# Performance work log

Hardware: AMD Instinct MI355X
Metric: run time of the kernel (lower is better)

Reference implementation:

```python
import jax, jax.numpy as jnp
import numpy as np

LEVELS = (4, 3, 2, 1)
EMBED = 4096


def _spp(x):
    # adaptive max pool to n x n per level (H,W divisible by every level), concat
    N, C, H, W = x.shape
    feats = []
    for n in LEVELS:
        p = x.reshape(N, C, n, H // n, n, W // n).max(axis=(3, 5))
        feats.append(p.reshape(N, C * n * n))
    return jnp.concatenate(feats, axis=1)  # (N, 90)


def _lstm_cell(x, h, c, wih, whh, bih, bhh):
    # torch gate order: i, f, g, o
    g = x @ wih.T + bih + h @ whh.T + bhh
    i, f, gg, o = jnp.split(g, 4, axis=-1)
    c2 = jax.nn.sigmoid(f) * c + jax.nn.sigmoid(i) * jnp.tanh(gg)
    h2 = jax.nn.sigmoid(o) * jnp.tanh(c2)
    return h2, c2


def _lin_init(key, out_d, in_d):
    k = 1.0 / np.sqrt(in_d)
    kw, kb = jax.random.split(key)
    w = jax.random.uniform(kw, (out_d, in_d), jnp.float32, -k, k)
    b = jax.random.uniform(kb, (out_d,), jnp.float32, -k, k)
    return w, b


def setup_inputs() -> dict:
    key = jax.random.key(0)
    ks = jax.random.split(key, 9)
    frames = jax.random.normal(ks[0], (8, 256, 3, 96, 96), jnp.float32)
    spp_fc_w, spp_fc_b = _lin_init(ks[1], EMBED, 90)
    fc7_w, fc7_b = _lin_init(ks[2], 64, EMBED)
    forecast_w, forecast_b = _lin_init(ks[3], 90, 32)
    fc8_w, fc8_b = _lin_init(ks[4], 1, 32)
    lstm1_wih, lstm1_bih = _lin_init(ks[5], 256, 64)
    lstm1_whh, lstm1_bhh = _lin_init(ks[6], 256, 64)
    lstm2_wih, lstm2_bih = _lin_init(ks[7], 128, 64)
    lstm2_whh, lstm2_bhh = _lin_init(ks[8], 128, 32)
    return dict(frames=frames, spp_fc_w=spp_fc_w, spp_fc_b=spp_fc_b,
                fc7_w=fc7_w, fc7_b=fc7_b,
                lstm1_wih=lstm1_wih, lstm1_whh=lstm1_whh, lstm1_bih=lstm1_bih, lstm1_bhh=lstm1_bhh,
                lstm2_wih=lstm2_wih, lstm2_whh=lstm2_whh, lstm2_bih=lstm2_bih, lstm2_bhh=lstm2_bhh,
                forecast_w=forecast_w, forecast_b=forecast_b, fc8_w=fc8_w, fc8_b=fc8_b)


def reference(frames, spp_fc_w, spp_fc_b, fc7_w, fc7_b,
              lstm1_wih, lstm1_whh, lstm1_bih, lstm1_bhh,
              lstm2_wih, lstm2_whh, lstm2_bih, lstm2_bhh,
              forecast_w, forecast_b, fc8_w, fc8_b):
    B, S, C, H, W = frames.shape
    pooled = _spp(frames.reshape(B * S, C, H, W))               # (B*S, 90)
    emb = jax.nn.relu(pooled @ spp_fc_w.T + spp_fc_b)           # (B*S, 4096)
    emb = jax.nn.relu(emb @ fc7_w.T + fc7_b).reshape(B, S, -1)  # (B, S, 64)

    def step(carry, e):
        h1, c1, h2, c2 = carry
        h1n, c1n = _lstm_cell(e, h1, c1, lstm1_wih, lstm1_whh, lstm1_bih, lstm1_bhh)
        h2n, c2n = _lstm_cell(h1n, h2, c2, lstm2_wih, lstm2_whh, lstm2_bih, lstm2_bhh)
        fpool = h2n @ forecast_w.T + forecast_b                  # (B, 90)
        fe = jax.nn.relu(fpool @ spp_fc_w.T + spp_fc_b)
        fe = jax.nn.relu(fe @ fc7_w.T + fc7_b)
        fh1, _ = _lstm_cell(fe, h1n, c1n, lstm1_wih, lstm1_whh, lstm1_bih, lstm1_bhh)
        fh2, _ = _lstm_cell(fh1, h2n, c2n, lstm2_wih, lstm2_whh, lstm2_bih, lstm2_bhh)
        return (h1n, c1n, h2n, c2n), (h2n, fh2, fpool)

    z = lambda d: jnp.zeros((B, d), frames.dtype)
    init = (z(64), z(64), z(32), z(32))
    _, (prog, fprog, fpooled) = jax.lax.scan(step, init, jnp.swapaxes(emb, 0, 1))
    prog = jnp.swapaxes(prog, 0, 1)        # (B, S, 32)
    fprog = jnp.swapaxes(fprog, 0, 1)      # (B, S, 32)
    fpooled = jnp.swapaxes(fpooled, 0, 1)  # (B, S, 90)
    progress = jax.nn.sigmoid(prog @ fc8_w.T + fc8_b)[..., 0]    # (B, S)
    fprogress = jax.nn.sigmoid(fprog @ fc8_w.T + fc8_b)[..., 0]  # (B, S)
    return (progress, fprogress, pooled.reshape(B, S, -1), fpooled)
```

## Files before the change

### kernel.cpp

```cpp
#include <hip/hip_runtime.h>
#include <math.h>

static const size_t OFF_POOLED = 0;
static const size_t OFF_EMB1   = 184320;
static const size_t OFF_ACC1   = OFF_EMB1 + 8388608;
static const size_t OFF_ACC2   = OFF_ACC1 + 131072;
static const size_t OFF_X1     = OFF_ACC2 + 131072;
static const size_t OFF_FPOOL  = OFF_X1 + 524288;
static const size_t OFF_H1     = OFF_FPOOL + 184320;
static const size_t OFF_C1     = OFF_H1 + 131072;
static const size_t OFF_H2     = OFF_C1 + 131072;
static const size_t OFF_C2     = OFF_H2 + 65536;

typedef _Float16 h2f_t __attribute__((ext_vector_type(2)));

__device__ __forceinline__ float fsig(float x) {
    return __builtin_amdgcn_rcpf(1.0f + __expf(-x));
}
__device__ __forceinline__ float ftanh(float x) {
    return 1.0f - 2.0f * __builtin_amdgcn_rcpf(__expf(2.0f * x) + 1.0f);
}

__device__ __forceinline__ float fdot2(h2f_t a, h2f_t b, float c) {
#if __has_builtin(__builtin_amdgcn_fdot2)
    return __builtin_amdgcn_fdot2(a, b, c, false);
#else
    return c + (float)a.x * (float)b.x + (float)a.y * (float)b.y;
#endif
}
__device__ __forceinline__ h2f_t h2pack(float x, float y) {
    h2f_t r; r.x = (_Float16)x; r.y = (_Float16)y; return r;
}
__device__ __forceinline__ h2f_t h2bits(int v) {
    return __builtin_bit_cast(h2f_t, v);
}
__device__ __forceinline__ void lds_fence() {
    asm volatile("s_waitcnt lgkmcnt(0)" ::: "memory");
}
__device__ __forceinline__ void permswap(float& x, float& y) {
    asm volatile("v_permlane32_swap_b32 %0, %1" : "+v"(x), "+v"(y));
}

__global__ __launch_bounds__(256) void spp_kernel(const float* __restrict__ frames,
                                                  float* __restrict__ out_pooled,
                                                  float* __restrict__ ws_pooled) {
    __shared__ __align__(16) float img[9216];
    __shared__ float p4[16], p3[9];
    int blk = blockIdx.x;
    int n = blk / 3, c = blk % 3;
    const float* src = frames + (size_t)blk * 9216;
    int tid = threadIdx.x;
    const float4* s4 = (const float4*)src;
    float4* i4 = (float4*)img;
#pragma unroll
    for (int j = 0; j < 9; ++j) i4[tid + 256 * j] = s4[tid + 256 * j];
    __syncthreads();
    {
        int r = tid >> 4, i = tid & 15;
        int ri = r >> 2, rj = r & 3;
        const float* base = &img[(24 * ri) * 96 + 24 * rj];
        float m = -3.402823466e38f;
#pragma unroll 6
        for (int k = 0; k < 36; ++k) {
            int e = i + 16 * k;
            int row = e / 24;
            int col = e - row * 24;
            m = fmaxf(m, base[row * 96 + col]);
        }
#pragma unroll
        for (int sh = 8; sh >= 1; sh >>= 1) m = fmaxf(m, __shfl_xor(m, sh));
        if (i == 0) p4[r] = m;
    }
    if (tid < 144) {
        int r = tid >> 4, i = tid & 15;
        int ri = r / 3, rj = r % 3;
        const float* base = &img[(32 * ri) * 96 + 32 * rj];
        float m = -3.402823466e38f;
#pragma unroll 8
        for (int k = 0; k < 64; ++k) {
            int e = i + 16 * k;
            int row = e >> 5, col = e & 31;
            m = fmaxf(m, base[row * 96 + col]);
        }
#pragma unroll
        for (int sh = 8; sh >= 1; sh >>= 1) m = fmaxf(m, __shfl_xor(m, sh));
        if (i == 0) p3[r] = m;
    }
    __syncthreads();
    if (tid < 30) {
        float v; int off;
        if (tid < 16) { v = p4[tid]; off = c * 16 + tid; }
        else if (tid < 25) { int q = tid - 16; v = p3[q]; off = 48 + c * 9 + q; }
        else if (tid < 29) {
            int q = tid - 25; int i2 = q >> 1, j2 = q & 1;
            v = fmaxf(fmaxf(p4[(2 * i2) * 4 + 2 * j2], p4[(2 * i2) * 4 + 2 * j2 + 1]),
                      fmaxf(p4[(2 * i2 + 1) * 4 + 2 * j2], p4[(2 * i2 + 1) * 4 + 2 * j2 + 1]));
            off = 75 + c * 4 + q;
        } else {
            float m = p4[0];
#pragma unroll
            for (int q = 1; q < 16; ++q) m = fmaxf(m, p4[q]);
            v = m; off = 87 + c;
        }
        out_pooled[(size_t)n * 90 + off] = v;
        ws_pooled[(size_t)n * 90 + off] = v;
    }
}

__global__ __launch_bounds__(256) void gemm90_kernel(const float* __restrict__ X,
                                                     const float* __restrict__ W,
                                                     const float* __restrict__ bias,
                                                     float* __restrict__ Y) {
    __shared__ __align__(16) float Xs[32][132];
    __shared__ __align__(16) float Ws[32][132];
    int tid = threadIdx.x;
    int R0 = blockIdx.x * 128, C0 = blockIdx.y * 128;
    int r0t = (tid >> 4) * 8, c0t = (tid & 15) * 8;
    float acc[8][8];
#pragma unroll
    for (int i = 0; i < 8; ++i)
// ... 68 lines not shown
    __shared__ __align__(16) float Xs[32][132];
    __shared__ __align__(16) float Ws[32][68];
    int tid = threadIdx.x;
    int R0 = blockIdx.x * 128;
    int K0 = blockIdx.y * 256;
    int r0t = (tid >> 4) * 8, c0t = (tid & 15) * 4;
    float acc[8][4];
#pragma unroll
    for (int i = 0; i < 8; ++i)
#pragma unroll
        for (int j = 0; j < 4; ++j) acc[i][j] = 0.f;

    for (int k0 = K0; k0 < K0 + 256; k0 += 32) {
#pragma unroll
        for (int j = 0; j < 4; ++j) {
            int idx = tid + 256 * j;
            int row = idx & 127, q = idx >> 7;
            float4 a = *(const float4*)&X[(size_t)(R0 + row) * 4096 + k0 + 4 * q];
            Xs[4 * q + 0][row] = a.x; Xs[4 * q + 1][row] = a.y;
            Xs[4 * q + 2][row] = a.z; Xs[4 * q + 3][row] = a.w;
        }
#pragma unroll
        for (int j = 0; j < 2; ++j) {
            int idx = tid + 256 * j;
            int col = idx & 63, q = idx >> 6;
            float4 a = *(const float4*)&W[(size_t)col * 4096 + k0 + 4 * q];
            Ws[4 * q + 0][col] = a.x; Ws[4 * q + 1][col] = a.y;
            Ws[4 * q + 2][col] = a.z; Ws[4 * q + 3][col] = a.w;
        }
        __syncthreads();
#pragma unroll 8
        for (int kk = 0; kk < 32; ++kk) {
            float4 xa = *(const float4*)&Xs[kk][r0t];
            float4 xb = *(const float4*)&Xs[kk][r0t + 4];
            float4 wa = *(const float4*)&Ws[kk][c0t];
            float xr[8] = {xa.x, xa.y, xa.z, xa.w, xb.x, xb.y, xb.z, xb.w};
            float wc[4] = {wa.x, wa.y, wa.z, wa.w};
#pragma unroll
            for (int i = 0; i < 8; ++i)
#pragma unroll
                for (int j = 0; j < 4; ++j) acc[i][j] += xr[i] * wc[j];
        }
        __syncthreads();
    }
#pragma unroll
    for (int i = 0; i < 8; ++i)
#pragma unroll
        for (int j = 0; j < 4; ++j)
            atomicAdd(&acc_out[(size_t)(R0 + r0t + i) * 64 + c0t + j], acc[i][j]);
}

__global__ __launch_bounds__(256) void x1_kernel(const float* __restrict__ acc1,
                                                 const float* __restrict__ fc7_b,
                                                 const float* __restrict__ wih1,
                                                 const float* __restrict__ bih1,
                                                 const float* __restrict__ bhh1,
                                                 float* __restrict__ X1) {
    __shared__ __align__(16) float xr[8][64];
    int tid = threadIdx.x;
    int R0 = blockIdx.x * 8;
#pragma unroll
    for (int j = 0; j < 2; ++j) {
        int idx = tid + 256 * j;
        int r = idx >> 6, k = idx & 63;
        xr[r][k] = fmaxf(acc1[(size_t)(R0 + r) * 64 + k] + fc7_b[k], 0.f);
    }
    __syncthreads();
    int u = tid;
    float w[64];
#pragma unroll
    for (int q = 0; q < 16; ++q) {
        float4 a = *(const float4*)&wih1[(size_t)u * 64 + 4 * q];
        w[4 * q] = a.x; w[4 * q + 1] = a.y; w[4 * q + 2] = a.z; w[4 * q + 3] = a.w;
    }
    float bias = bih1[u] + bhh1[u];
    for (int r = 0; r < 8; ++r) {
        float g = bias;
#pragma unroll
        for (int k = 0; k < 64; ++k) g += w[k] * xr[r][k];
        X1[(size_t)(R0 + r) * 256 + u] = g;
    }
}

__global__ __launch_bounds__(128, 1) void seq_kernel(const float* __restrict__ X1,
                                                     const float* __restrict__ whh1,
                                                     const float* __restrict__ wih2,
                                                     const float* __restrict__ whh2,
                                                     const float* __restrict__ bih2,
                                                     const float* __restrict__ bhh2,
                                                     float* __restrict__ h1_all, float* __restrict__ c1_all,
                                                     float* __restrict__ h2_all, float* __restrict__ c2_all) {
    __shared__ __align__(16) _Float16 h1h[2][64];
    __shared__ __align__(16) _Float16 h2h[32];
    const int tid = threadIdx.x;
    const int l = tid & 63;
    const size_t n0 = (size_t)blockIdx.x * 256;
    const float* xp = X1 + n0 * 256;

    if (tid < 64) {
        h2f_t w1[4][32];
#pragma unroll
        for (int g = 0; g < 4; ++g) {
            const float* wr = whh1 + (size_t)(g * 64 + l) * 64;
#pragma unroll
            for (int q = 0; q < 32; ++q) w1[g][q] = h2pack(wr[2 * q], wr[2 * q + 1]);
        }
        float c1;
        {
            float a0 = xp[l], a1 = xp[64 + l], a2 = xp[128 + l], a3 = xp[192 + l];
            (void)a1;
            c1 = fsig(a0) * ftanh(a2);
            float h1n = fsig(a3) * ftanh(c1);
            h1h[0][l] = (_Float16)h1n;
            h1_all[n0 * 64 + l] = h1n;
            c1_all[n0 * 64 + l] = c1;
        }
        float xb0[4], xb1[4];
        {
            const float* x1r = xp + 256;
            xb0[0] = x1r[l]; xb0[1] = x1r[64 + l]; xb0[2] = x1r[128 + l]; xb0[3] = x1r[192 + l];
            const float* x2r = xp + 512;
            xb1[0] = x2r[l]; xb1[1] = x2r[64 + l]; xb1[2] = x2r[128 + l]; xb1[3] = x2r[192 + l];
        }
        lds_fence();
        int4 hv[8];
        {
            const int4* hb = (const int4*)&h1h[0][0];
#pragma unroll
            for (int q = 0; q < 8; ++q) hv[q] = hb[q];
        }
        __builtin_amdgcn_s_barrier();

#pragma unroll 2
        for (int t = 0; t < 256; ++t) {
            float* xc = (t & 1) ? xb1 : xb0;
            float a0 = xc[0], a1 = xc[1], a2 = xc[2], a3 = xc[3];
            {
                int tr = (t + 3 < 256) ? (t + 3) : 255;
                const float* xq = xp + (size_t)tr * 256;
                xc[0] = xq[l]; xc[1] = xq[64 + l]; xc[2] = xq[128 + l]; xc[3] = xq[192 + l];
            }
            float b0 = 0.f, b1 = 0.f, b2 = 0.f, b3 = 0.f;
#pragma unroll
            for (int q = 0; q < 8; ++q) {
                int4 v = hv[q];
                h2f_t hh0 = h2bits(v.x), hh1 = h2bits(v.y), hh2 = h2bits(v.z), hh3 = h2bits(v.w);
                a0 = fdot2(w1[0][4 * q], hh0, a0);     a1 = fdot2(w1[1][4 * q], hh0, a1);
                a2 = fdot2(w1[2][4 * q], hh0, a2);     a3 = fdot2(w1[3][4 * q], hh0, a3);
                b0 = fdot2(w1[0][4 * q + 1], hh1, b0); b1 = fdot2(w1[1][4 * q + 1], hh1, b1);
                b2 = fdot2(w1[2][4 * q + 1], hh1, b2); b3 = fdot2(w1[3][4 * q + 1], hh1, b3);
                a0 = fdot2(w1[0][4 * q + 2], hh2, a0); a1 = fdot2(w1[1][4 * q + 2], hh2, a1);
                a2 = fdot2(w1[2][4 * q + 2], hh2, a2); a3 = fdot2(w1[3][4 * q + 2], hh2, a3);
                b0 = fdot2(w1[0][4 * q + 3], hh3, b0); b1 = fdot2(w1[1][4 * q + 3], hh3, b1);
                b2 = fdot2(w1[2][4 * q + 3], hh3, b2); b3 = fdot2(w1[3][4 * q + 3], hh3, b3);
            }
            a0 += b0; a1 += b1; a2 += b2; a3 += b3;
            c1 = fsig(a1) * c1 + fsig(a0) * ftanh(a2);
            float h1n = fsig(a3) * ftanh(c1);
            h1h[(t + 1) & 1][l] = (_Float16)h1n;
            if (t < 255) {
                h1_all[(n0 + t + 1) * 64 + l] = h1n;
                c1_all[(n0 + t + 1) * 64 + l] = c1;
            }
            {
                const int4* hb = (const int4*)&h1h[(t + 1) & 1][0];
#pragma unroll
                for (int q = 0; q < 8; ++q) hv[q] = hb[q];
            }
            asm volatile("s_waitcnt lgkmcnt(8)" ::: "memory");
            __builtin_amdgcn_s_barrier();
        }
    } else {
        h2f_t w2a[2][32], w2b[2][16];
#pragma unroll
        for (int g = 0; g < 2; ++g) {
            const float* wa = wih2 + (size_t)(g * 64 + l) * 64;
#pragma unroll
            for (int q = 0; q < 32; ++q) w2a[g][q] = h2pack(wa[2 * q], wa[2 * q + 1]);
            const float* wb = whh2 + (size_t)(g * 64 + l) * 32;
#pragma unroll
            for (int q = 0; q < 16; ++q) w2b[g][q] = h2pack(wb[2 * q], wb[2 * q + 1]);
        }
        const float b2a = bih2[l] + bhh2[l];
        const float b2b = bih2[64 + l] + bhh2[64 + l];
        const bool hi = (l >= 32);
        if (l < 32) h2h[l] = (_Float16)0.f;
        lds_fence();
        int4 gv[4];
        {
            const int4* gb = (const int4*)&h2h[0];
#pragma unroll
            for (int q = 0; q < 4; ++q) gv[q] = gb[q];
        }
        float c2 = 0.f;
        __builtin_amdgcn_s_barrier();

        for (int t = 0; t < 256; ++t) {
            int4 hv[8];
            {
                const int4* hb = (const int4*)&h1h[t & 1][0];
#pragma unroll
                for (int q = 0; q < 8; ++q) hv[q] = hb[q];
            }
            float pa = b2a, pb = b2b, pc = 0.f, pd = 0.f;
            float pe = 0.f, pf = 0.f, pg = 0.f, ph = 0.f;
#pragma unroll
            for (int q = 0; q < 4; ++q) {
                int4 u = gv[q];
                h2f_t gg0 = h2bits(u.x), gg1 = h2bits(u.y), gg2 = h2bits(u.z), gg3 = h2bits(u.w);
                pe = fdot2(w2b[0][4 * q], gg0, pe);     pf = fdot2(w2b[1][4 * q], gg0, pf);
                pg = fdot2(w2b[0][4 * q + 1], gg1, pg); ph = fdot2(w2b[1][4 * q + 1], gg1, ph);
                pe = fdot2(w2b[0][4 * q + 2], gg2, pe); pf = fdot2(w2b[1][4 * q + 2], gg2, pf);
                pg = fdot2(w2b[0][4 * q + 3], gg3, pg); ph = fdot2(w2b[1][4 * q + 3], gg3, ph);
            }
#pragma unroll
            for (int q = 0; q < 8; ++q) {
                int4 v = hv[q];
                h2f_t hh0 = h2bits(v.x), hh1 = h2bits(v.y), hh2 = h2bits(v.z), hh3 = h2bits(v.w);
                pa = fdot2(w2a[0][4 * q], hh0, pa);     pb = fdot2(w2a[1][4 * q], hh0, pb);
                pa = fdot2(w2a[0][4 * q + 1], hh1, pa); pb = fdot2(w2a[1][4 * q + 1], hh1, pb);
                pc = fdot2(w2a[0][4 * q + 2], hh2, pc); pd = fdot2(w2a[1][4 * q + 2], hh2, pd);
                pc = fdot2(w2a[0][4 * q + 3], hh3, pc); pd = fdot2(w2a[1][4 * q + 3], hh3, pd);
            }
            pa = (pa + pc) + (pe + pg);
            pb = (pb + pd) + (pf + ph);
            float s1a = pa, s1b = pb;
            permswap(s1a, s1b);
            float s2a = pb, s2b = pa;
            permswap(s2a, s2b);
            float gi = hi ? s2a : s1a;
            float gf = hi ? s2b : s1b;
            float gg = hi ? s1a : s2a;
            float go = hi ? s1b : s2b;
            c2 = fsig(gf) * c2 + fsig(gi) * ftanh(gg);
            float h2n = fsig(go) * ftanh(c2);
            if (l < 32) {
                h2h[l] = (_Float16)h2n;
                h2_all[(n0 + t) * 32 + l] = h2n;
                c2_all[(n0 + t) * 32 + l] = c2;
            }
            lds_fence();
            {
                const int4* gb = (const int4*)&h2h[0];
#pragma unroll
                for (int q = 0; q < 4; ++q) gv[q] = gb[q];
            }
            __builtin_amdgcn_s_barrier();
        }
    }
}

__global__ __launch_bounds__(256) void fpool_kernel(const float* __restrict__ h2_all,
                                                    const float* __restrict__ fw,
                                                    const float* __restrict__ fb,
                                                    const float* __restrict__ fc8_w,
                                                    const float* __restrict__ fc8_b,
                                                    float* __restrict__ fpool_ws,
                                                    float* __restrict__ out_fpooled,
                                                    float* __restrict__ out_progress) {
    __shared__ __align__(16) float h2t[16][32];
    __shared__ float fwl[2880];
    int tid = threadIdx.x;
    int R0 = blockIdx.x * 16;
#pragma unroll
    for (int j = 0; j < 2; ++j) {
        int idx = tid + 256 * j;
        int r = idx >> 5, k = idx & 31;
        h2t[r][k] = h2_all[(size_t)(R0 + r) * 32 + k];
    }
    for (int idx = tid; idx < 2880; idx += 256) fwl[idx] = fw[idx];
    __syncthreads();
    for (int j = 0; j < 6; ++j) {
        int idx = tid + 256 * j;
        if (idx < 1440) {
            int r = idx / 90, cc = idx % 90;
            float g = fb[cc];
#pragma unroll
            for (int k = 0; k < 32; ++k) g += h2t[r][k] * fwl[cc * 32 + k];
            fpool_ws[(size_t)(R0 + r) * 90 + cc] = g;
            out_fpooled[(size_t)(R0 + r) * 90 + cc] = g;
        }
    }
    if (tid < 16) {
        float g = fc8_b[0];
#pragma unroll
        for (int k = 0; k < 32; ++k) g += h2t[tid][k] * fc8_w[k];
        out_progress[R0 + tid] = fsig(g);
    }
}

__global__ __launch_bounds__(256) void fh_kernel(const float* __restrict__ acc2,
                                                 const float* __restrict__ fc7_b,
                                                 const float* __restrict__ h1_all,
                                                 const float* __restrict__ c1_all,
                                                 const float* __restrict__ h2_all,
                                                 const float* __restrict__ c2_all,
                                                 const float* __restrict__ wih1,
                                                 const float* __restrict__ whh1,
                                                 const float* __restrict__ bih1,
                                                 const float* __restrict__ bhh1,
                                                 const float* __restrict__ wih2,
                                                 const float* __restrict__ whh2,
                                                 const float* __restrict__ bih2,
                                                 const float* __restrict__ bhh2,
                                                 const float* __restrict__ fc8_w,
                                                 const float* __restrict__ fc8_b,
                                                 float* __restrict__ out_fprog) {
    __shared__ __align__(16) float xcat[8][128];
    __shared__ float g1f[8][256];
    __shared__ __align__(16) float x2c[8][96];
    __shared__ float g2f[8][128];
    __shared__ __align__(16) float fh2s[8][32];
    int tid = threadIdx.x;
    int R0 = blockIdx.x * 8;
#pragma unroll
    for (int j = 0; j < 4; ++j) {
        int idx = tid + 256 * j;
        int r = idx >> 7, k = idx & 127;
        float v;
        if (k < 64) v = fmaxf(acc2[(size_t)(R0 + r) * 64 + k] + fc7_b[k], 0.f);
        else v = h1_all[(size_t)(R0 + r) * 64 + (k - 64)];
        xcat[r][k] = v;
    }
    {
        int r = tid >> 5, k = tid & 31;
        x2c[r][64 + k] = h2_all[(size_t)(R0 + r) * 32 + k];
    }
    __syncthreads();
    {
        int u = tid;
// ... 32 lines not shown
        float wa[64], wb2[32];
#pragma unroll
        for (int q = 0; q < 16; ++q) {
            float4 a = *(const float4*)&wih2[(size_t)u * 64 + 4 * q];
            wa[4 * q] = a.x; wa[4 * q + 1] = a.y; wa[4 * q + 2] = a.z; wa[4 * q + 3] = a.w;
        }
#pragma unroll
        for (int q = 0; q < 8; ++q) {
            float4 b = *(const float4*)&whh2[(size_t)u * 32 + 4 * q];
            wb2[4 * q] = b.x; wb2[4 * q + 1] = b.y; wb2[4 * q + 2] = b.z; wb2[4 * q + 3] = b.w;
        }
        float bias = bih2[u] + bhh2[u];
        for (int r = rb; r < rb + 4; ++r) {
            float g = bias;
#pragma unroll
            for (int k = 0; k < 64; ++k) g += wa[k] * x2c[r][k];
#pragma unroll
            for (int k = 0; k < 32; ++k) g += wb2[k] * x2c[r][64 + k];
            g2f[r][u] = g;
        }
    }
    __syncthreads();
    {
        int r = tid >> 5, v = tid & 31;
        float gi = g2f[r][v], gf = g2f[r][32 + v], gg = g2f[r][64 + v], go = g2f[r][96 + v];
        float c2v = c2_all[(size_t)(R0 + r) * 32 + v];
        float c = fsig(gf) * c2v + fsig(gi) * ftanh(gg);
        fh2s[r][v] = fsig(go) * ftanh(c);
    }
    __syncthreads();
    if (tid < 8) {
        float g = fc8_b[0];
#pragma unroll
        for (int k = 0; k < 32; ++k) g += fh2s[tid][k] * fc8_w[k];
        out_fprog[R0 + tid] = fsig(g);
    }
}

extern "C" void kernel_launch(void* const* d_in, const int* in_sizes, int n_in,
                              void* d_out, int out_size, void* d_ws, size_t ws_size,
                              hipStream_t stream) {
    (void)in_sizes; (void)n_in; (void)out_size; (void)ws_size;
    const float* frames   = (const float*)d_in[0];
    const float* spp_fc_w = (const float*)d_in[1];
    const float* spp_fc_b = (const float*)d_in[2];
    const float* fc7_w    = (const float*)d_in[3];
    const float* fc7_b    = (const float*)d_in[4];
    const float* l1_wih   = (const float*)d_in[5];
    const float* l1_whh   = (const float*)d_in[6];
    const float* l1_bih   = (const float*)d_in[7];
    const float* l1_bhh   = (const float*)d_in[8];
    const float* l2_wih   = (const float*)d_in[9];
    const float* l2_whh   = (const float*)d_in[10];
    const float* l2_bih   = (const float*)d_in[11];
    const float* l2_bhh   = (const float*)d_in[12];
    const float* fo_w     = (const float*)d_in[13];
    const float* fo_b     = (const float*)d_in[14];
    const float* fc8_w    = (const float*)d_in[15];
    const float* fc8_b    = (const float*)d_in[16];
    float* out = (float*)d_out;
    float* ws  = (float*)d_ws;

    float* pooled = ws + OFF_POOLED;
    float* emb1   = ws + OFF_EMB1;
    float* acc1   = ws + OFF_ACC1;
    float* acc2   = ws + OFF_ACC2;
    float* X1     = ws + OFF_X1;
    float* fpool  = ws + OFF_FPOOL;
    float* h1a    = ws + OFF_H1;
    float* c1a    = ws + OFF_C1;
    float* h2a    = ws + OFF_H2;
    float* c2a    = ws + OFF_C2;

    float* out_prog    = out;
    float* out_fprog   = out + 2048;
    float* out_pooled  = out + 4096;
    float* out_fpooled = out + 188416;

    hipMemsetAsync(acc1, 0, (size_t)262144 * sizeof(float), stream);
    spp_kernel<<<6144, 256, 0, stream>>>(frames, out_pooled, pooled);
    gemm90_kernel<<<dim3(16, 32), 256, 0, stream>>>(pooled, spp_fc_w, spp_fc_b, emb1);
    gemmk_kernel<<<dim3(16, 16), 256, 0, stream>>>(emb1, fc7_w, acc1);
    x1_kernel<<<256, 256, 0, stream>>>(acc1, fc7_b, l1_wih, l1_bih, l1_bhh, X1);
    seq_kernel<<<8, 128, 0, stream>>>(X1, l1_whh, l2_wih, l2_whh, l2_bih, l2_bhh, h1a, c1a, h2a, c2a);
    fpool_kernel<<<128, 256, 0, stream>>>(h2a, fo_w, fo_b, fc8_w, fc8_b, fpool, out_fpooled, out_prog);
    gemm90_kernel<<<dim3(16, 32), 256, 0, stream>>>(fpool, spp_fc_w, spp_fc_b, emb1);
    gemmk_kernel<<<dim3(16, 16), 256, 0, stream>>>(emb1, fc7_w, acc2);
    fh_kernel<<<256, 256, 0, stream>>>(acc2, fc7_b, h1a, c1a, h2a, c2a,
                                       l1_wih, l1_whh, l1_bih, l1_bhh,
                                       l2_wih, l2_whh, l2_bih, l2_bhh,
                                       fc8_w, fc8_b, out_fprog);
}
```

Before: 669.5 us.

## Split LSTM recurrence dot products across four waves with LDS partial sums

Result: slower. 723.9 us (+8.1%).

```diff
diff --git a/kernel.cpp b/kernel.cpp
--- a/kernel.cpp
+++ b/kernel.cpp
@@ -270,7 +270,7 @@
     }
 }
 
-__global__ __launch_bounds__(128, 1) void seq_kernel(const float* __restrict__ X1,
+__global__ __launch_bounds__(256, 1) void seq_kernel(const float* __restrict__ X1,
                                                      const float* __restrict__ whh1,
                                                      const float* __restrict__ wih2,
                                                      const float* __restrict__ whh2,
@@ -280,23 +280,25 @@
                                                      float* __restrict__ h2_all, float* __restrict__ c2_all) {
     __shared__ __align__(16) _Float16 h1h[2][64];
     __shared__ __align__(16) _Float16 h2h[32];
+    __shared__ __align__(16) float p1[64][4];
+    __shared__ __align__(16) float p2[64][2];
     const int tid = threadIdx.x;
+    const int wid = tid >> 6;
     const int l = tid & 63;
     const size_t n0 = (size_t)blockIdx.x * 256;
     const float* xp = X1 + n0 * 256;
 
-    if (tid < 64) {
-        h2f_t w1[4][32];
+    if (wid == 0) {
+        h2f_t w1c[4][12];
 #pragma unroll
         for (int g = 0; g < 4; ++g) {
             const float* wr = whh1 + (size_t)(g * 64 + l) * 64;
 #pragma unroll
-            for (int q = 0; q < 32; ++q) w1[g][q] = h2pack(wr[2 * q], wr[2 * q + 1]);
+            for (int q = 0; q < 12; ++q) w1c[g][q] = h2pack(wr[2 * q], wr[2 * q + 1]);
         }
         float c1;
         {
-            float a0 = xp[l], a1 = xp[64 + l], a2 = xp[128 + l], a3 = xp[192 + l];
-            (void)a1;
+            float a0 = xp[l], a2 = xp[128 + l], a3 = xp[192 + l];
             c1 = fsig(a0) * ftanh(a2);
             float h1n = fsig(a3) * ftanh(c1);
             h1h[0][l] = (_Float16)h1n;
@@ -311,14 +313,13 @@
             xb1[0] = x2r[l]; xb1[1] = x2r[64 + l]; xb1[2] = x2r[128 + l]; xb1[3] = x2r[192 + l];
         }
         lds_fence();
-        int4 hv[8];
+        __builtin_amdgcn_s_barrier();
+        int4 hv[3];
         {
             const int4* hb = (const int4*)&h1h[0][0];
 #pragma unroll
-            for (int q = 0; q < 8; ++q) hv[q] = hb[q];
-        }
-        __builtin_amdgcn_s_barrier();
-
+            for (int q = 0; q < 3; ++q) hv[q] = hb[q];
+        }
 #pragma unroll 2
         for (int t = 0; t < 256; ++t) {
             float* xc = (t & 1) ? xb1 : xb0;
@@ -330,19 +331,21 @@
             }
             float b0 = 0.f, b1 = 0.f, b2 = 0.f, b3 = 0.f;
 #pragma unroll
-            for (int q = 0; q < 8; ++q) {
+            for (int q = 0; q < 3; ++q) {
                 int4 v = hv[q];
                 h2f_t hh0 = h2bits(v.x), hh1 = h2bits(v.y), hh2 = h2bits(v.z), hh3 = h2bits(v.w);
-                a0 = fdot2(w1[0][4 * q], hh0, a0);     a1 = fdot2(w1[1][4 * q], hh0, a1);
-                a2 = fdot2(w1[2][4 * q], hh0, a2);     a3 = fdot2(w1[3][4 * q], hh0, a3);
-                b0 = fdot2(w1[0][4 * q + 1], hh1, b0); b1 = fdot2(w1[1][4 * q + 1], hh1, b1);
-                b2 = fdot2(w1[2][4 * q + 1], hh1, b2); b3 = fdot2(w1[3][4 * q + 1], hh1, b3);
-                a0 = fdot2(w1[0][4 * q + 2], hh2, a0); a1 = fdot2(w1[1][4 * q + 2], hh2, a1);
-                a2 = fdot2(w1[2][4 * q + 2], hh2, a2); a3 = fdot2(w1[3][4 * q + 2], hh2, a3);
-                b0 = fdot2(w1[0][4 * q + 3], hh3, b0); b1 = fdot2(w1[1][4 * q + 3], hh3, b1);
-                b2 = fdot2(w1[2][4 * q + 3], hh3, b2); b3 = fdot2(w1[3][4 * q + 3], hh3, b3);
-            }
-            a0 += b0; a1 += b1; a2 += b2; a3 += b3;
+                a0 = fdot2(w1c[0][4 * q], hh0, a0);     a1 = fdot2(w1c[1][4 * q], hh0, a1);
+                a2 = fdot2(w1c[2][4 * q], hh0, a2);     a3 = fdot2(w1c[3][4 * q], hh0, a3);
+                b0 = fdot2(w1c[0][4 * q + 1], hh1, b0); b1 = fdot2(w1c[1][4 * q + 1], hh1, b1);
+                b2 = fdot2(w1c[2][4 * q + 1], hh1, b2); b3 = fdot2(w1c[3][4 * q + 1], hh1, b3);
+                a0 = fdot2(w1c[0][4 * q + 2], hh2, a0); a1 = fdot2(w1c[1][4 * q + 2], hh2, a1);
+                a2 = fdot2(w1c[2][4 * q + 2], hh2, a2); a3 = fdot2(w1c[3][4 * q + 2], hh2, a3);
+                b0 = fdot2(w1c[0][4 * q + 3], hh3, b0); b1 = fdot2(w1c[1][4 * q + 3], hh3, b1);
+                b2 = fdot2(w1c[2][4 * q + 3], hh3, b2); b3 = fdot2(w1c[3][4 * q + 3], hh3, b3);
+            }
+            __builtin_amdgcn_s_barrier();
+            float4 p = *(const float4*)&p1[l][0];
+            a0 += b0 + p.x; a1 += b1 + p.y; a2 += b2 + p.z; a3 += b3 + p.w;
             c1 = fsig(a1) * c1 + fsig(a0) * ftanh(a2);
             float h1n = fsig(a3) * ftanh(c1);
             h1h[(t + 1) & 1][l] = (_Float16)h1n;
@@ -353,65 +356,93 @@
             {
                 const int4* hb = (const int4*)&h1h[(t + 1) & 1][0];
 #pragma unroll
-                for (int q = 0; q < 8; ++q) hv[q] = hb[q];
-            }
-            asm volatile("s_waitcnt lgkmcnt(8)" ::: "memory");
+                for (int q = 0; q < 3; ++q) hv[q] = hb[q];
+            }
+            asm volatile("s_waitcnt lgkmcnt(3)" ::: "memory");
             __builtin_amdgcn_s_barrier();
         }
-    } else {
-        h2f_t w2a[2][32], w2b[2][16];
+    } else if (wid == 1) {
+        h2f_t w1c[4][20];
+#pragma unroll
+        for (int g = 0; g < 4; ++g) {
+            const float* wr = whh1 + (size_t)(g * 64 + l) * 64 + 24;
+#pragma unroll
+            for (int q = 0; q < 20; ++q) w1c[g][q] = h2pack(wr[2 * q], wr[2 * q + 1]);
+        }
+        __builtin_amdgcn_s_barrier();
+        int4 hv[5];
+        {
+            const int4* hb = (const int4*)&h1h[0][0];
+#pragma unroll
+            for (int q = 0; q < 5; ++q) hv[q] = hb[q + 3];
+        }
+        for (int t = 0; t < 256; ++t) {
+            float a0 = 0.f, a1 = 0.f, a2 = 0.f, a3 = 0.f;
+            float b0 = 0.f, b1 = 0.f, b2 = 0.f, b3 = 0.f;
+#pragma unroll
+            for (int q = 0; q < 5; ++q) {
+                int4 v = hv[q];
+                h2f_t hh0 = h2bits(v.x), hh1 = h2bits(v.y), hh2 = h2bits(v.z), hh3 = h2bits(v.w);
+                a0 = fdot2(w1c[0][4 * q], hh0, a0);     a1 = fdot2(w1c[1][4 * q], hh0, a1);
+                a2 = fdot2(w1c[2][4 * q], hh0, a2);     a3 = fdot2(w1c[3][4 * q], hh0, a3);
+                b0 = fdot2(w1c[0][4 * q + 1], hh1, b0); b1 = fdot2(w1c[1][4 * q + 1], hh1, b1);
+                b2 = fdot2(w1c[2][4 * q + 1], hh1, b2); b3 = fdot2(w1c[3][4 * q + 1], hh1, b3);
+                a0 = fdot2(w1c[0][4 * q + 2], hh2, a0); a1 = fdot2(w1c[1][4 * q + 2], hh2, a1);
+                a2 = fdot2(w1c[2][4 * q + 2], hh2, a2); a3 = fdot2(w1c[3][4 * q + 2], hh2, a3);
+                b0 = fdot2(w1c[0][4 * q + 3], hh3, b0); b1 = fdot2(w1c[1][4 * q + 3], hh3, b1);
+                b2 = fdot2(w1c[2][4 * q + 3], hh3, b2); b3 = fdot2(w1c[3][4 * q + 3], hh3, b3);
+            }
+            float4 pw;
+            pw.x = a0 + b0; pw.y = a1 + b1; pw.z = a2 + b2; pw.w = a3 + b3;
+            *(float4*)&p1[l][0] = pw;
+            lds_fence();
+            __builtin_amdgcn_s_barrier();
+            __builtin_amdgcn_s_barrier();
+            {
+                const int4* hb = (const int4*)&h1h[(t + 1) & 1][0];
+#pragma unroll
+                for (int q = 0; q < 5; ++q) hv[q] = hb[q + 3];
+            }
+        }
+    } else if (wid == 2) {
+        h2f_t w2a[2][4], w2b[2][4];
 #pragma unroll
         for (int g = 0; g < 2; ++g) {
             const float* wa = wih2 + (size_t)(g * 64 + l) * 64;
 #pragma unroll
-            for (int q = 0; q < 32; ++q) w2a[g][q] = h2pack(wa[2 * q], wa[2 * q + 1]);
+            for (int q = 0; q < 4; ++q) w2a[g][q] = h2pack(wa[2 * q], wa[2 * q + 1]);
             const float* wb = whh2 + (size_t)(g * 64 + l) * 32;
 #pragma unroll
-            for (int q = 0; q < 16; ++q) w2b[g][q] = h2pack(wb[2 * q], wb[2 * q + 1]);
+            for (int q = 0; q < 4; ++q) w2b[g][q] = h2pack(wb[2 * q], wb[2 * q + 1]);
         }
         const float b2a = bih2[l] + bhh2[l];
         const float b2b = bih2[64 + l] + bhh2[64 + l];
         const bool hi = (l >= 32);
-        if (l < 32) h2h[l] = (_Float16)0.f;
-        lds_fence();
-        int4 gv[4];
-        {
-            const int4* gb = (const int4*)&h2h[0];
-#pragma unroll
-            for (int q = 0; q < 4; ++q) gv[q] = gb[q];
-        }
         float c2 = 0.f;
+        int4 gv; gv.x = 0; gv.y = 0; gv.z = 0; gv.w = 0;
         __builtin_amdgcn_s_barrier();
-
+        int4 hv = ((const int4*)&h1h[0][0])[0];
         for (int t = 0; t < 256; ++t) {
-            int4 hv[8];
+            float pe = 0.f, pf = 0.f, pg_ = 0.f, ph = 0.f;
             {
-                const int4* hb = (const int4*)&h1h[t & 1][0];
-#pragma unroll
-                for (int q = 0; q < 8; ++q) hv[q] = hb[q];
+                h2f_t gg0 = h2bits(gv.x), gg1 = h2bits(gv.y), gg2 = h2bits(gv.z), gg3 = h2bits(gv.w);
+                pe = fdot2(w2b[0][0], gg0, pe);  pf = fdot2(w2b[1][0], gg0, pf);
+                pg_ = fdot2(w2b[0][1], gg1, pg_); ph = fdot2(w2b[1][1], gg1, ph);
+                pe = fdot2(w2b[0][2], gg2, pe);  pf = fdot2(w2b[1][2], gg2, pf);
+                pg_ = fdot2(w2b[0][3], gg3, pg_); ph = fdot2(w2b[1][3], gg3, ph);
             }
             float pa = b2a, pb = b2b, pc = 0.f, pd = 0.f;
-            float pe = 0.f, pf = 0.f, pg = 0.f, ph = 0.f;
-#pragma unroll
-            for (int q = 0; q < 4; ++q) {
-                int4 u = gv[q];
-                h2f_t gg0 = h2bits(u.x), gg1 = h2bits(u.y), gg2 = h2bits(u.z), gg3 = h2bits(u.w);
-                pe = fdot2(w2b[0][4 * q], gg0, pe);     pf = fdot2(w2b[1][4 * q], gg0, pf);
-                pg = fdot2(w2b[0][4 * q + 1], gg1, pg); ph = fdot2(w2b[1][4 * q + 1], gg1, ph);
-                pe = fdot2(w2b[0][4 * q + 2], gg2, pe); pf = fdot2(w2b[1][4 * q + 2], gg2, pf);
-                pg = fdot2(w2b[0][4 * q + 3], gg3, pg); ph = fdot2(w2b[1][4 * q + 3], gg3, ph);
-            }
-#pragma unroll
-            for (int q = 0; q < 8; ++q) {
-                int4 v = hv[q];
-                h2f_t hh0 = h2bits(v.x), hh1 = h2bits(v.y), hh2 = h2bits(v.z), hh3 = h2bits(v.w);
-                pa = fdot2(w2a[0][4 * q], hh0, pa);     pb = fdot2(w2a[1][4 * q], hh0, pb);
-                pa = fdot2(w2a[0][4 * q + 1], hh1, pa); pb = fdot2(w2a[1][4 * q + 1], hh1, pb);
-                pc = fdot2(w2a[0][4 * q + 2], hh2, pc); pd = fdot2(w2a[1][4 * q + 2], hh2, pd);
-                pc = fdot2(w2a[0][4 * q + 3], hh3, pc); pd = fdot2(w2a[1][4 * q + 3], hh3, pd);
-            }
-            pa = (pa + pc) + (pe + pg);
-            pb = (pb + pd) + (pf + ph);
+            {
+                h2f_t hh0 = h2bits(hv.x), hh1 = h2bits(hv.y), hh2 = h2bits(hv.z), hh3 = h2bits(hv.w);
+                pa = fdot2(w2a[0][0], hh0, pa); pb = fdot2(w2a[1][0], hh0, pb);
+                pa = fdot2(w2a[0][1], hh1, pa); pb = fdot2(w2a[1][1], hh1, pb);
+                pc = fdot2(w2a[0][2], hh2, pc); pd = fdot2(w2a[1][2], hh2, pd);
+                pc = fdot2(w2a[0][3], hh3, pc); pd = fdot2(w2a[1][3], hh3, pd);
+            }
+            __builtin_amdgcn_s_barrier();
+            float2 q2 = *(const float2*)&p2[l][0];
+            pa = ((pa + pc) + (pe + pg_)) + q2.x;
+            pb = ((pb + pd) + (pf + ph)) + q2.y;
             float s1a = pa, s1b = pb;
             permswap(s1a, s1b);
             float s2a = pb, s2b = pa;
@@ -427,13 +458,68 @@
                 h2_all[(n0 + t) * 32 + l] = h2n;
                 c2_all[(n0 + t) * 32 + l] = c2;
             }
+            gv = ((const int4*)&h2h[0])[0];
+            asm volatile("s_waitcnt lgkmcnt(1)" ::: "memory");
+            __builtin_amdgcn_s_barrier();
+            hv = ((const int4*)&h1h[(t + 1) & 1][0])[0];
+        }
+    } else {
+        h2f_t w2a[2][28], w2b[2][12];
+#pragma unroll
+        for (int g = 0; g < 2; ++g) {
+            const float* wa = wih2 + (size_t)(g * 64 + l) * 64 + 8;
+#pragma unroll
+            for (int q = 0; q < 28; ++q) w2a[g][q] = h2pack(wa[2 * q], wa[2 * q + 1]);
+            const float* wb = whh2 + (size_t)(g * 64 + l) * 32 + 8;
+#pragma unroll
+            for (int q = 0; q < 12; ++q) w2b[g][q] = h2pack(wb[2 * q], wb[2 * q + 1]);
+        }
+        int4 gv[3];
+#pragma unroll
+        for (int q = 0; q < 3; ++q) { gv[q].x = 0; gv[q].y = 0; gv[q].z = 0; gv[q].w = 0; }
+        __builtin_amdgcn_s_barrier();
+        int4 hv[7];
+        {
+            const int4* hb = (const int4*)&h1h[0][0];
+#pragma unroll
+            for (int q = 0; q < 7; ++q) hv[q] = hb[q + 1];
+        }
+        for (int t = 0; t < 256; ++t) {
+            float re = 0.f, rf = 0.f, rg = 0.f, rh = 0.f;
+#pragma unroll
+            for (int q = 0; q < 3; ++q) {
+                int4 u = gv[q];
+                h2f_t gg0 = h2bits(u.x), gg1 = h2bits(u.y), gg2 = h2bits(u.z), gg3 = h2bits(u.w);
+                re = fdot2(w2b[0][4 * q], gg0, re);     rf = fdot2(w2b[1][4 * q], gg0, rf);
+                rg = fdot2(w2b[0][4 * q + 1], gg1, rg); rh = fdot2(w2b[1][4 * q + 1], gg1, rh);
+                re = fdot2(w2b[0][4 * q + 2], gg2, re); rf = fdot2(w2b[1][4 * q + 2], gg2, rf);
+                rg = fdot2(w2b[0][4 * q + 3], gg3, rg); rh = fdot2(w2b[1][4 * q + 3], gg3, rh);
+            }
+            float ra = 0.f, rb = 0.f, rc = 0.f, rd = 0.f;
+#pragma unroll
+            for (int q = 0; q < 7; ++q) {
+                int4 v = hv[q];
+                h2f_t hh0 = h2bits(v.x), hh1 = h2bits(v.y), hh2 = h2bits(v.z), hh3 = h2bits(v.w);
+                ra = fdot2(w2a[0][4 * q], hh0, ra);     rb = fdot2(w2a[1][4 * q], hh0, rb);
+                ra = fdot2(w2a[0][4 * q + 1], hh1, ra); rb = fdot2(w2a[1][4 * q + 1], hh1, rb);
+                rc = fdot2(w2a[0][4 * q + 2], hh2, rc); rd = fdot2(w2a[1][4 * q + 2], hh2, rd);
+                rc = fdot2(w2a[0][4 * q + 3], hh3, rc); rd = fdot2(w2a[1][4 * q + 3], hh3, rd);
+            }
+            float2 pw;
+            pw.x = (ra + rc) + (re + rg);
+            pw.y = (rb + rd) + (rf + rh);
+            *(float2*)&p2[l][0] = pw;
             lds_fence();
+            __builtin_amdgcn_s_barrier();
+            __builtin_amdgcn_s_barrier();
             {
                 const int4* gb = (const int4*)&h2h[0];
 #pragma unroll
-                for (int q = 0; q < 4; ++q) gv[q] = gb[q];
-            }
-            __builtin_amdgcn_s_barrier();
+                for (int q = 0; q < 3; ++q) gv[q] = gb[q + 1];
+                const int4* hb = (const int4*)&h1h[(t + 1) & 1][0];
+#pragma unroll
+                for (int q = 0; q < 7; ++q) hv[q] = hb[q + 1];
+            }
         }
     }
 }
@@ -632,7 +718,7 @@
     gemm90_kernel<<<dim3(16, 32), 256, 0, stream>>>(pooled, spp_fc_w, spp_fc_b, emb1);
     gemmk_kernel<<<dim3(16, 16), 256, 0, stream>>>(emb1, fc7_w, acc1);
     x1_kernel<<<256, 256, 0, stream>>>(acc1, fc7_b, l1_wih, l1_bih, l1_bhh, X1);
-    seq_kernel<<<8, 128, 0, stream>>>(X1, l1_whh, l2_wih, l2_whh, l2_bih, l2_bhh, h1a, c1a, h2a, c2a);
+    seq_kernel<<<8, 256, 0, stream>>>(X1, l1_whh, l2_wih, l2_whh, l2_bih, l2_bhh, h1a, c1a, h2a, c2a);
     fpool_kernel<<<128, 256, 0, stream>>>(h2a, fo_w, fo_b, fc8_w, fc8_b, fpool, out_fpooled, out_prog);
     gemm90_kernel<<<dim3(16, 32), 256, 0, stream>>>(fpool, spp_fc_w, spp_fc_b, emb1);
     gemmk_kernel<<<dim3(16, 16), 256, 0, stream>>>(emb1, fc7_w, acc2);
```

## Split sequential LSTM recurrence across four waves per block

Applied to the files above, without the earlier changes.

New measurement: 842.2 us. 1.26x slower.

```diff
diff --git a/kernel.cpp b/kernel.cpp
--- a/kernel.cpp
+++ b/kernel.cpp
@@ -36,6 +36,14 @@
 }
 __device__ __forceinline__ void lds_fence() {
     asm volatile("s_waitcnt lgkmcnt(0)" ::: "memory");
+}
+__device__ __forceinline__ float swz_xor1(float x) {
+    return __builtin_bit_cast(float,
+        __builtin_amdgcn_ds_swizzle(__builtin_bit_cast(int, x), 0x041F));
+}
+__device__ __forceinline__ float swz_xor16(float x) {
+    return __builtin_bit_cast(float,
+        __builtin_amdgcn_ds_swizzle(__builtin_bit_cast(int, x), 0x401F));
 }
 __device__ __forceinline__ void permswap(float& x, float& y) {
     asm volatile("v_permlane32_swap_b32 %0, %1" : "+v"(x), "+v"(y));
@@ -270,7 +278,7 @@
     }
 }
 
-__global__ __launch_bounds__(128, 1) void seq_kernel(const float* __restrict__ X1,
+__global__ __launch_bounds__(256, 1) void seq_kernel(const float* __restrict__ X1,
                                                      const float* __restrict__ whh1,
                                                      const float* __restrict__ wih2,
                                                      const float* __restrict__ whh2,
@@ -279,108 +287,122 @@
                                                      float* __restrict__ h1_all, float* __restrict__ c1_all,
                                                      float* __restrict__ h2_all, float* __restrict__ c2_all) {
     __shared__ __align__(16) _Float16 h1h[2][64];
-    __shared__ __align__(16) _Float16 h2h[32];
+    __shared__ __align__(16) _Float16 h2h[2][32];
     const int tid = threadIdx.x;
+    const int wid = tid >> 6;
     const int l = tid & 63;
     const size_t n0 = (size_t)blockIdx.x * 256;
     const float* xp = X1 + n0 * 256;
 
-    if (tid < 64) {
-        h2f_t w1[4][32];
-#pragma unroll
-        for (int g = 0; g < 4; ++g) {
-            const float* wr = whh1 + (size_t)(g * 64 + l) * 64;
-#pragma unroll
-            for (int q = 0; q < 32; ++q) w1[g][q] = h2pack(wr[2 * q], wr[2 * q + 1]);
+    if (wid < 2) {
+        const int w = wid;
+        const int j = l >> 1, p = l & 1;
+        const int u = 32 * w + j;
+        const int rA = p ? 64 + u : u;
+        const int rB = p ? 192 + u : 128 + u;
+        h2f_t wA[32], wB[32];
+#pragma unroll
+        for (int q = 0; q < 32; ++q) {
+            wA[q] = h2pack(whh1[(size_t)rA * 64 + 2 * q], whh1[(size_t)rA * 64 + 2 * q + 1]);
+            wB[q] = h2pack(whh1[(size_t)rB * 64 + 2 * q], whh1[(size_t)rB * 64 + 2 * q + 1]);
         }
         float c1;
         {
-            float a0 = xp[l], a1 = xp[64 + l], a2 = xp[128 + l], a3 = xp[192 + l];
-            (void)a1;
-            c1 = fsig(a0) * ftanh(a2);
-            float h1n = fsig(a3) * ftanh(c1);
-            h1h[0][l] = (_Float16)h1n;
-            h1_all[n0 * 64 + l] = h1n;
-            c1_all[n0 * 64 + l] = c1;
-        }
-        float xb0[4], xb1[4];
-        {
-            const float* x1r = xp + 256;
-            xb0[0] = x1r[l]; xb0[1] = x1r[64 + l]; xb0[2] = x1r[128 + l]; xb0[3] = x1r[192 + l];
-            const float* x2r = xp + 512;
-            xb1[0] = x2r[l]; xb1[1] = x2r[64 + l]; xb1[2] = x2r[128 + l]; xb1[3] = x2r[192 + l];
-        }
-        lds_fence();
+            float xi = xp[u], xg = xp[128 + u], xo = xp[192 + u];
+            c1 = fsig(xi) * ftanh(xg);
+            float h1n = fsig(xo) * ftanh(c1);
+            if (p == 0) {
+                h1h[0][u] = (_Float16)h1n;
+                h1_all[n0 * 64 + u] = h1n;
+                c1_all[n0 * 64 + u] = c1;
+            }
+        }
+        float xA0 = xp[256 + rA], xB0 = xp[256 + rB];
+        float xA1 = xp[512 + rA], xB1 = xp[512 + rB];
         int4 hv[8];
         {
             const int4* hb = (const int4*)&h1h[0][0];
 #pragma unroll
-            for (int q = 0; q < 8; ++q) hv[q] = hb[q];
-        }
+            for (int q = 0; q < 4; ++q) hv[4 * w + q] = hb[4 * w + q];
+        }
+        lds_fence();
         __builtin_amdgcn_s_barrier();
+        {
+            const int4* hb = (const int4*)&h1h[0][0];
+            const int o = 4 * (1 - w);
+#pragma unroll
+            for (int q = 0; q < 4; ++q) hv[o + q] = hb[o + q];
+        }
 
 #pragma unroll 2
         for (int t = 0; t < 256; ++t) {
-            float* xc = (t & 1) ? xb1 : xb0;
-            float a0 = xc[0], a1 = xc[1], a2 = xc[2], a3 = xc[3];
+            float xAc = (t & 1) ? xA1 : xA0;
+            float xBc = (t & 1) ? xB1 : xB0;
             {
                 int tr = (t + 3 < 256) ? (t + 3) : 255;
-                const float* xq = xp + (size_t)tr * 256;
-                xc[0] = xq[l]; xc[1] = xq[64 + l]; xc[2] = xq[128 + l]; xc[3] = xq[192 + l];
-            }
-            float b0 = 0.f, b1 = 0.f, b2 = 0.f, b3 = 0.f;
+                float nA = xp[(size_t)tr * 256 + rA];
+                float nB = xp[(size_t)tr * 256 + rB];
+                if (t & 1) { xA1 = nA; xB1 = nB; } else { xA0 = nA; xB0 = nB; }
+            }
+            float a0 = xAc, a1 = 0.f, a2 = 0.f, a3 = 0.f;
+            float b0 = xBc, b1 = 0.f, b2 = 0.f, b3 = 0.f;
 #pragma unroll
             for (int q = 0; q < 8; ++q) {
                 int4 v = hv[q];
-                h2f_t hh0 = h2bits(v.x), hh1 = h2bits(v.y), hh2 = h2bits(v.z), hh3 = h2bits(v.w);
-                a0 = fdot2(w1[0][4 * q], hh0, a0);     a1 = fdot2(w1[1][4 * q], hh0, a1);
-                a2 = fdot2(w1[2][4 * q], hh0, a2);     a3 = fdot2(w1[3][4 * q], hh0, a3);
-                b0 = fdot2(w1[0][4 * q + 1], hh1, b0); b1 = fdot2(w1[1][4 * q + 1], hh1, b1);
-                b2 = fdot2(w1[2][4 * q + 1], hh1, b2); b3 = fdot2(w1[3][4 * q + 1], hh1, b3);
-                a0 = fdot2(w1[0][4 * q + 2], hh2, a0); a1 = fdot2(w1[1][4 * q + 2], hh2, a1);
-                a2 = fdot2(w1[2][4 * q + 2], hh2, a2); a3 = fdot2(w1[3][4 * q + 2], hh2, a3);
-                b0 = fdot2(w1[0][4 * q + 3], hh3, b0); b1 = fdot2(w1[1][4 * q + 3], hh3, b1);
-                b2 = fdot2(w1[2][4 * q + 3], hh3, b2); b3 = fdot2(w1[3][4 * q + 3], hh3, b3);
-            }
-            a0 += b0; a1 += b1; a2 += b2; a3 += b3;
-            c1 = fsig(a1) * c1 + fsig(a0) * ftanh(a2);
-            float h1n = fsig(a3) * ftanh(c1);
-            h1h[(t + 1) & 1][l] = (_Float16)h1n;
-            if (t < 255) {
-                h1_all[(n0 + t + 1) * 64 + l] = h1n;
-                c1_all[(n0 + t + 1) * 64 + l] = c1;
+                h2f_t h0 = h2bits(v.x), h1_ = h2bits(v.y), h2_ = h2bits(v.z), h3 = h2bits(v.w);
+                a0 = fdot2(wA[4 * q],     h0,  a0); b0 = fdot2(wB[4 * q],     h0,  b0);
+                a1 = fdot2(wA[4 * q + 1], h1_, a1); b1 = fdot2(wB[4 * q + 1], h1_, b1);
+                a2 = fdot2(wA[4 * q + 2], h2_, a2); b2 = fdot2(wB[4 * q + 2], h2_, b2);
+                a3 = fdot2(wA[4 * q + 3], h3,  a3); b3 = fdot2(wB[4 * q + 3], h3,  b3);
+            }
+            float sA = (a0 + a1) + (a2 + a3);
+            float sB = (b0 + b1) + (b2 + b3);
+            float swA = swz_xor1(sA);
+            float swB = swz_xor1(sB);
+            float gi = p ? swA : sA;
+            float gf = p ? sA : swA;
+            float gg = p ? swB : sB;
+            float go = p ? sB : swB;
+            c1 = fsig(gf) * c1 + fsig(gi) * ftanh(gg);
+            float h1n = fsig(go) * ftanh(c1);
+            if (p == 0) {
+                h1h[(t + 1) & 1][u] = (_Float16)h1n;
+                if (t < 255) {
+                    h1_all[(n0 + t + 1) * 64 + u] = h1n;
+                    c1_all[(n0 + t + 1) * 64 + u] = c1;
+                }
             }
             {
                 const int4* hb = (const int4*)&h1h[(t + 1) & 1][0];
 #pragma unroll
-                for (int q = 0; q < 8; ++q) hv[q] = hb[q];
-            }
-            asm volatile("s_waitcnt lgkmcnt(8)" ::: "memory");
+                for (int q = 0; q < 4; ++q) hv[4 * w + q] = hb[4 * w + q];
+            }
+            asm volatile("s_waitcnt lgkmcnt(4)" ::: "memory");
             __builtin_amdgcn_s_barrier();
+            {
+                const int4* hb = (const int4*)&h1h[(t + 1) & 1][0];
+                const int o = 4 * (1 - w);
+#pragma unroll
+                for (int q = 0; q < 4; ++q) hv[o + q] = hb[o + q];
+            }
         }
     } else {
-        h2f_t w2a[2][32], w2b[2][16];
-#pragma unroll
-        for (int g = 0; g < 2; ++g) {
-            const float* wa = wih2 + (size_t)(g * 64 + l) * 64;
-#pragma unroll
-            for (int q = 0; q < 32; ++q) w2a[g][q] = h2pack(wa[2 * q], wa[2 * q + 1]);
-            const float* wb = whh2 + (size_t)(g * 64 + l) * 32;
-#pragma unroll
-            for (int q = 0; q < 16; ++q) w2b[g][q] = h2pack(wb[2 * q], wb[2 * q + 1]);
-        }
-        const float b2a = bih2[l] + bhh2[l];
-        const float b2b = bih2[64 + l] + bhh2[64 + l];
-        const bool hi = (l >= 32);
-        if (l < 32) h2h[l] = (_Float16)0.f;
+        const int w2 = wid - 2;
+        const int g = l >> 4, j = l & 15;
+        const int v = 16 * w2 + j;
+        const int row = 32 * g + v;
+        h2f_t wa[32], wb[16];
+#pragma unroll
+        for (int q = 0; q < 32; ++q)
+            wa[q] = h2pack(wih2[(size_t)row * 64 + 2 * q], wih2[(size_t)row * 64 + 2 * q + 1]);
+#pragma unroll
+        for (int q = 0; q < 16; ++q)
+            wb[q] = h2pack(whh2[(size_t)row * 32 + 2 * q], whh2[(size_t)row * 32 + 2 * q + 1]);
+        const float bias = bih2[row] + bhh2[row];
+        const bool lo = (l < 32);
+        float c2 = 0.f;
+        if (w2 == 0 && l < 32) h2h[0][l] = (_Float16)0.f;
         lds_fence();
-        int4 gv[4];
-        {
-            const int4* gb = (const int4*)&h2h[0];
-#pragma unroll
-            for (int q = 0; q < 4; ++q) gv[q] = gb[q];
-        }
-        float c2 = 0.f;
         __builtin_amdgcn_s_barrier();
 
         for (int t = 0; t < 256; ++t) {
@@ -390,49 +412,49 @@
 #pragma unroll
                 for (int q = 0; q < 8; ++q) hv[q] = hb[q];
             }
-            float pa = b2a, pb = b2b, pc = 0.f, pd = 0.f;
-            float pe = 0.f, pf = 0.f, pg = 0.f, ph = 0.f;
-#pragma unroll
-            for (int q = 0; q < 4; ++q) {
-                int4 u = gv[q];
-                h2f_t gg0 = h2bits(u.x), gg1 = h2bits(u.y), gg2 = h2bits(u.z), gg3 = h2bits(u.w);
-                pe = fdot2(w2b[0][4 * q], gg0, pe);     pf = fdot2(w2b[1][4 * q], gg0, pf);
-                pg = fdot2(w2b[0][4 * q + 1], gg1, pg); ph = fdot2(w2b[1][4 * q + 1], gg1, ph);
-                pe = fdot2(w2b[0][4 * q + 2], gg2, pe); pf = fdot2(w2b[1][4 * q + 2], gg2, pf);
-                pg = fdot2(w2b[0][4 * q + 3], gg3, pg); ph = fdot2(w2b[1][4 * q + 3], gg3, ph);
-            }
+            int4 gv[2];
+            {
+                const int4* gb = (const int4*)&h2h[t & 1][0];
+                gv[0] = gb[0]; gv[1] = gb[1];
+            }
+            float s4 = 0.f, s5 = 0.f, s6 = 0.f, s7 = 0.f;
+#pragma unroll
+            for (int q = 0; q < 2; ++q) {
+                int4 uq = gv[q];
+                h2f_t g0 = h2bits(uq.x), g1 = h2bits(uq.y), g2 = h2bits(uq.z), g3 = h2bits(uq.w);
+                s4 = fdot2(wb[8 * q],     g0, s4); s5 = fdot2(wb[8 * q + 1], g1, s5);
+                s6 = fdot2(wb[8 * q + 2], g2, s6); s7 = fdot2(wb[8 * q + 3], g3, s7);
+                s4 = fdot2(wb[8 * q + 4], g0, s4); s5 = fdot2(wb[8 * q + 5], g1, s5);
+                s6 = fdot2(wb[8 * q + 6], g2, s6); s7 = fdot2(wb[8 * q + 7], g3, s7);
+            }
+            float s0 = bias, s1 = 0.f, s2 = 0.f, s3 = 0.f;
 #pragma unroll
             for (int q = 0; q < 8; ++q) {
-                int4 v = hv[q];
-                h2f_t hh0 = h2bits(v.x), hh1 = h2bits(v.y), hh2 = h2bits(v.z), hh3 = h2bits(v.w);
-                pa = fdot2(w2a[0][4 * q], hh0, pa);     pb = fdot2(w2a[1][4 * q], hh0, pb);
-                pa = fdot2(w2a[0][4 * q + 1], hh1, pa); pb = fdot2(w2a[1][4 * q + 1], hh1, pb);
-                pc = fdot2(w2a[0][4 * q + 2], hh2, pc); pd = fdot2(w2a[1][4 * q + 2], hh2, pd);
-                pc = fdot2(w2a[0][4 * q + 3], hh3, pc); pd = fdot2(w2a[1][4 * q + 3], hh3, pd);
-            }
-            pa = (pa + pc) + (pe + pg);
-            pb = (pb + pd) + (pf + ph);
-            float s1a = pa, s1b = pb;
-            permswap(s1a, s1b);
-            float s2a = pb, s2b = pa;
-            permswap(s2a, s2b);
-            float gi = hi ? s2a : s1a;
-            float gf = hi ? s2b : s1b;
-            float gg = hi ? s1a : s2a;
-            float go = hi ? s1b : s2b;
+                int4 vq = hv[q];
+                h2f_t h0 = h2bits(vq.x), h1_ = h2bits(vq.y), h2_ = h2bits(vq.z), h3 = h2bits(vq.w);
+                s0 = fdot2(wa[4 * q],     h0,  s0); s1 = fdot2(wa[4 * q + 1], h1_, s1);
+                s2 = fdot2(wa[4 * q + 2], h2_, s2); s3 = fdot2(wa[4 * q + 3], h3,  s3);
+            }
+            float s = ((s0 + s1) + (s2 + s3)) + ((s4 + s5) + (s6 + s7));
+            float t1 = swz_xor16(s);
+            float X1v = (g & 1) ? t1 : s;
+            float X2v = (g & 1) ? s : t1;
+            float a_ = X1v, b_ = X2v;
+            permswap(a_, b_);
+            float c_ = X2v, d_ = X1v;
+            permswap(c_, d_);
+            float gi = lo ? a_ : c_;
+            float gf = lo ? c_ : a_;
+            float gg = lo ? b_ : d_;
+            float go = lo ? d_ : b_;
             c2 = fsig(gf) * c2 + fsig(gi) * ftanh(gg);
             float h2n = fsig(go) * ftanh(c2);
-            if (l < 32) {
-                h2h[l] = (_Float16)h2n;
-                h2_all[(n0 + t) * 32 + l] = h2n;
-                c2_all[(n0 + t) * 32 + l] = c2;
+            if (g == 0) {
+                h2h[(t + 1) & 1][v] = (_Float16)h2n;
+                h2_all[(n0 + t) * 32 + v] = h2n;
+                c2_all[(n0 + t) * 32 + v] = c2;
             }
             lds_fence();
-            {
-                const int4* gb = (const int4*)&h2h[0];
-#pragma unroll
-                for (int q = 0; q < 4; ++q) gv[q] = gb[q];
-            }
             __builtin_amdgcn_s_barrier();
         }
     }
@@ -632,7 +654,7 @@
     gemm90_kernel<<<dim3(16, 32), 256, 0, stream>>>(pooled, spp_fc_w, spp_fc_b, emb1);
     gemmk_kernel<<<dim3(16, 16), 256, 0, stream>>>(emb1, fc7_w, acc1);
     x1_kernel<<<256, 256, 0, stream>>>(acc1, fc7_b, l1_wih, l1_bih, l1_bhh, X1);
-    seq_kernel<<<8, 128, 0, stream>>>(X1, l1_whh, l2_wih, l2_whh, l2_bih, l2_bhh, h1a, c1a, h2a, c2a);
+    seq_kernel<<<8, 256, 0, stream>>>(X1, l1_whh, l2_wih, l2_whh, l2_bih, l2_bhh, h1a, c1a, h2a, c2a);
     fpool_kernel<<<128, 256, 0, stream>>>(h2a, fo_w, fo_b, fc8_w, fc8_b, fpool, out_fpooled, out_prog);
     gemm90_kernel<<<dim3(16, 32), 256, 0, stream>>>(fpool, spp_fc_w, spp_fc_b, emb1);
     gemmk_kernel<<<dim3(16, 16), 256, 0, stream>>>(emb1, fc7_w, acc2);
```
